# Kernel optimization log

Measured on AMD Instinct MI355X. Metric: run time of the kernel, lower is better.

The kernel has to match this reference:

```python
import jax, jax.numpy as jnp
import numpy as np

GN_GROUPS = 32
GN_EPS = 1e-5


def _conv3x3(x, w, b):
    # NCHW 3x3 conv, stride 1, pad 1
    y = jax.lax.conv_general_dilated(x, w, (1, 1), [(1, 1), (1, 1)],
                                     dimension_numbers=('NCHW', 'OIHW', 'NCHW'))
    return y + b[None, :, None, None]


def _bilinear(x, py, px):
    # x: [N,C,H,W]; py,px: [N,H,W] fractional sample coords; zeros outside.
    N, C, H, W = x.shape
    y0 = jnp.floor(py)
    x0 = jnp.floor(px)
    wy = py - y0
    wx = px - x0
    xf = x.reshape(N, C, H * W)
    out = jnp.zeros((N, C, H, W), x.dtype)
    corners = ((y0, x0, (1 - wy) * (1 - wx)),
               (y0, x0 + 1, (1 - wy) * wx),
               (y0 + 1, x0, wy * (1 - wx)),
               (y0 + 1, x0 + 1, wy * wx))
    for yy, xx, w in corners:
        valid = ((yy >= 0) & (yy <= H - 1) & (xx >= 0) & (xx <= W - 1)).astype(x.dtype)
        yi = jnp.clip(yy, 0, H - 1).astype(jnp.int32)
        xi = jnp.clip(xx, 0, W - 1).astype(jnp.int32)
        idx = (yi * W + xi).reshape(N, 1, H * W)
        g = jnp.take_along_axis(xf, idx, axis=2).reshape(N, C, H, W)
        out = out + g * (w * valid)[:, None]
    return out


def setup_inputs() -> dict:
    key = jax.random.key(0)
    ks = jax.random.split(key, 8)
    N, C, H, W = 4, 128, 160, 160
    s = 0.05
    return {
        'x': jax.random.normal(ks[0], (N, C, H, W), jnp.float32),
        'w_tm': jax.random.normal(ks[1], (4, C, 3, 3), jnp.float32) * s,
        'b_tm': jax.random.normal(ks[2], (4,), jnp.float32) * s,
        'w_tr': jax.random.normal(ks[3], (2, C, 3, 3), jnp.float32) * s,
        'b_tr': jax.random.normal(ks[4], (2,), jnp.float32) * s,
        'w_dcn': jax.random.normal(ks[5], (C, C, 3, 3), jnp.float32) * s,
        'gn_gamma': jnp.ones((C,), jnp.float32),
        'gn_beta': jnp.zeros((C,), jnp.float32),
    }


def reference(x, w_tm, b_tm, w_tr, b_tr, w_dcn, gn_gamma, gn_beta):
    N, C, H, W = x.shape
    Cout = w_dcn.shape[0]
    # regular 3x3 grid offsets: row0 = ky, row1 = kx, k ordered ky-major
    R = jnp.array([[-1., -1., -1., 0., 0., 0., 1., 1., 1.],
                   [-1., 0., 1., -1., 0., 1., -1., 0., 1.]], x.dtype)
    tm = _conv3x3(x, w_tm, b_tm)   # [N,4,H,W] -> per-pixel 2x2 affine
    tr = _conv3x3(x, w_tr, b_tr)   # [N,2,H,W] -> per-pixel (dy,dx) translation
    tmm = tm.transpose(0, 2, 3, 1).reshape(N, H, W, 2, 2)
    off = jnp.einsum('nhwij,jk->nhwik', tmm, R) - R  # [N,H,W,2,9]
    dy = off[:, :, :, 0, :] + tr[:, 0][..., None]    # [N,H,W,9]
    dx = off[:, :, :, 1, :] + tr[:, 1][..., None]
    hh = jnp.arange(H, dtype=x.dtype)[None, :, None, None]
    ww = jnp.arange(W, dtype=x.dtype)[None, None, :, None]
    kk = jnp.arange(9)
    ky = (kk // 3).astype(x.dtype)
    kx = (kk % 3).astype(x.dtype)
    py = hh - 1.0 + ky + dy  # stride=1, pad=1, dilation=1
    px = ww - 1.0 + kx + dx
    wk = w_dcn.reshape(Cout, C, 9)
    out = jnp.zeros((N, Cout, H, W), x.dtype)
    for k in range(9):  # fixed small loop over kernel points
        s = _bilinear(x, py[..., k], px[..., k])
        out = out + jnp.einsum('nchw,oc->nohw', s, wk[:, :, k])
    # GroupNorm
    og = out.reshape(N, GN_GROUPS, (Cout // GN_GROUPS) * H * W)
    mu = og.mean(axis=2, keepdims=True)
    var = og.var(axis=2, keepdims=True)
    og = (og - mu) * jax.lax.rsqrt(var + GN_EPS)
    out = og.reshape(N, Cout, H, W) * gn_gamma[None, :, None, None] + gn_beta[None, :, None, None]
    return jax.nn.relu(out + x)
```

## Files before the change

### kernel.cpp

```cpp
#include <hip/hip_runtime.h>
#include <hip/hip_fp16.h>
#include <math.h>

#define Hh 160
#define Ww 160
#define Cc 128
#define HW 25600
#define NPIX 102400

typedef __attribute__((ext_vector_type(8))) _Float16 half8;
typedef __attribute__((ext_vector_type(4))) float f32x4;
typedef __attribute__((ext_vector_type(4))) unsigned int u32x4;

union h2u { __half2 h; unsigned int u; };

#define WS_OFFS 0u
#define WS_WA   7372800u
#define WS_GSUM 7667712u
#define WS_GSQ  7668224u
#define WS_XT   7668736u
#define WS_RAW  33883136u

__global__ void wtrans_kernel(const float* __restrict__ w_dcn,
                              unsigned short* __restrict__ wA) {
    int idx = blockIdx.x * 256 + threadIdx.x;
    if (idx >= 9 * 128 * 128) return;
    int k = idx >> 14;
    int o = (idx >> 7) & 127;
    int c = idx & 127;
    wA[idx] = __half_as_ushort(__float2half(w_dcn[(o * 128 + c) * 9 + k]));
}

__global__ void __launch_bounds__(256) xpose_kernel(
    const float* __restrict__ x, unsigned short* __restrict__ xT) {
    __shared__ float L[128 * 65];
    int b = blockIdx.x;
    int n = b / 400;
    int px0 = (b - n * 400) * 64;
    int t = threadIdx.x;
    const float* xn = x + (size_t)n * Cc * HW + px0;
#pragma unroll
    for (int i = 0; i < 32; ++i) {
        int idx = i * 256 + t;
        int ch = idx >> 6;
        int pxl = idx & 63;
        L[ch * 65 + pxl] = xn[(size_t)ch * HW + pxl];
    }
    __syncthreads();
    unsigned short* dst = xT + ((size_t)n * HW + px0) * 128;
#pragma unroll
    for (int j = 0; j < 16; ++j) {
        int idx = j * 256 + t;
        int pxl = idx >> 6;
        int cp = idx & 63;
        h2u cv;
        cv.h = __floats2half2_rn(L[(2 * cp) * 65 + pxl],
                                 L[(2 * cp + 1) * 65 + pxl]);
        *(unsigned int*)(dst + (size_t)pxl * 128 + cp * 2) = cv.u;
    }
}

__global__ void __launch_bounds__(256) offs_kernel(
    const float* __restrict__ x, const float* __restrict__ w_tm,
    const float* __restrict__ b_tm, const float* __restrict__ w_tr,
    const float* __restrict__ b_tr, float* __restrict__ offs2) {
    __shared__ float wt[128 * 9 * 8];
    int t = threadIdx.x;
    for (int idx = t; idx < 6912; idx += 256) {
        int j = idx % 6;
        int rest = idx / 6;
        int tap = rest % 9;
        int c = rest / 9;
        float v = (j < 4) ? w_tm[(j * 128 + c) * 9 + tap]
                          : w_tr[((j - 4) * 128 + c) * 9 + tap];
        wt[rest * 8 + j] = v;
    }
    __syncthreads();
    int bid = blockIdx.x;
    int blk = (bid & 7) * 50 + (bid >> 3);
    int p = blk * 256 + t;
    int n = p / HW;
    int hw = p - n * HW;
    int h = hw / Ww;
    int w = hw - h * Ww;
    int addr[9];
    float msk[9];
#pragma unroll
    for (int tap = 0; tap < 9; ++tap) {
        int dy = tap / 3 - 1, dx = tap % 3 - 1;
        int yy = h + dy, xx = w + dx;
        bool v = (yy >= 0) && (yy < Hh) && (xx >= 0) && (xx < Ww);
        addr[tap] = v ? yy * Ww + xx : 0;
        msk[tap] = v ? 1.f : 0.f;
    }
    float a0 = 0, a1 = 0, a2 = 0, a3 = 0, a4 = 0, a5 = 0;
    const float* xn = x + n * Cc * HW;
#pragma unroll 2
    for (int c = 0; c < Cc; ++c) {
        const float* xc = xn + c * HW;
#pragma unroll
        for (int tap = 0; tap < 9; ++tap) {
            float v = msk[tap] * xc[addr[tap]];
            const float* wp = &wt[(c * 9 + tap) * 8];
            float4 w4 = *(const float4*)wp;
            float2 w2 = *(const float2*)(wp + 4);
            a0 += v * w4.x; a1 += v * w4.y; a2 += v * w4.z; a3 += v * w4.w;
            a4 += v * w2.x; a5 += v * w2.y;
        }
    }
    a0 += b_tm[0]; a1 += b_tm[1]; a2 += b_tm[2]; a3 += b_tm[3];
    a4 += b_tr[0]; a5 += b_tr[1];
#pragma unroll
    for (int k = 0; k < 9; ++k) {
        float r0 = (float)(k / 3) - 1.f;
        float r1 = (float)(k % 3) - 1.f;
        float2 st;
        st.x = (float)h + a0 * r0 + a1 * r1 + a4;
        st.y = (float)w + a2 * r0 + a3 * r1 + a5;
        *(float2*)(offs2 + ((size_t)k * NPIX + p) * 2) = st;
    }
}

__global__ void __launch_bounds__(256, 2) dcn2_kernel(
    const unsigned short* __restrict__ xT, const float* __restrict__ offs2,
    const unsigned short* __restrict__ wA, float* __restrict__ raw,
    float* __restrict__ gsum, float* __restrict__ gsq) {
    __shared__ __align__(16) unsigned short Bt[128 * 128];
    int t = threadIdx.x;
    int lane = t & 63;
    int wid = t >> 6;
    int wm = wid & 1, wn = wid >> 1;
    int quad = lane >> 4, l15 = lane & 15;
    int sub = lane >> 4;
    int s = lane & 15;

    int bid = blockIdx.x;
    int blk = (bid & 7) * 100 + (bid >> 3);
    int px0 = blk * 128;
    int n = px0 / HW;
    int hw0 = px0 - n * HW;
    const unsigned short* xb = xT + (size_t)n * HW * 128;
    const char* Ag = (const char*)wA;
    const float2* offv = (const float2*)offs2;
    int pbase = px0 + wid * 32 + sub;
    int sb = s << 3;

    f32x4 acc[4][4];
#pragma unroll
    for (int i = 0; i < 4; ++i)
#pragma unroll
        for (int j = 0; j < 4; ++j) acc[i][j] = (f32x4)0.f;

    float2 pc[8];
#pragma unroll
    for (int r = 0; r < 8; ++r)
        pc[r] = offv[(size_t)0 * NPIX + pbase + r * 4];

    for (int k = 0; k < 9; ++k) {
        __syncthreads();

        float2 pcn[8];
        if (k < 8) {
#pragma unroll
            for (int r = 0; r < 8; ++r)
                pcn[r] = offv[(size_t)(k + 1) * NPIX + pbase + r * 4];
        }

#pragma unroll
        for (int r = 0; r < 8; ++r) {
            int p = wid * 32 + r * 4 + sub;
            float py = pc[r].x, pxx = pc[r].y;
            float y0f = floorf(py), x0f = floorf(pxx);
            float fy = py - y0f, fx = pxx - x0f;
            int y0 = (int)y0f, xi0 = (int)x0f;
            int y1 = y0 + 1, xi1 = xi0 + 1;
            float w00 = (1.f - fy) * (1.f - fx), w01 = (1.f - fy) * fx;
            float w10 = fy * (1.f - fx), w11 = fy * fx;
            bool vy0 = (unsigned)y0 < (unsigned)Hh;
            bool vy1 = (unsigned)y1 < (unsigned)Hh;
            bool vx0 = (unsigned)xi0 < (unsigned)Ww;
            bool vx1 = (unsigned)xi1 < (unsigned)Ww;
            w00 = (vy0 && vx0) ? w00 : 0.f;
            w01 = (vy0 && vx1) ? w01 : 0.f;
            w10 = (vy1 && vx0) ? w10 : 0.f;
            w11 = (vy1 && vx1) ? w11 : 0.f;
            int cy0 = vy0 ? y0 : 0, cy1 = vy1 ? y1 : 0;
            int cx0 = vx0 ? xi0 : 0, cx1 = vx1 ? xi1 : 0;
            u32x4 v00 = *(const u32x4*)(xb + ((size_t)(cy0 * Ww + cx0) << 7) + sb);
            u32x4 v01 = *(const u32x4*)(xb + ((size_t)(cy0 * Ww + cx1) << 7) + sb);
            u32x4 v10 = *(const u32x4*)(xb + ((size_t)(cy1 * Ww + cx0) << 7) + sb);
            u32x4 v11 = *(const u32x4*)(xb + ((size_t)(cy1 * Ww + cx1) << 7) + sb);
            __half2 W00 = __float2half2_rn(w00);
            __half2 W01 = __float2half2_rn(w01);
            __half2 W10 = __float2half2_rn(w10);
            __half2 W11 = __float2half2_rn(w11);
            u32x4 outv;
#pragma unroll
            for (int e = 0; e < 4; ++e) {
                h2u a, b, c, d, o;
                a.u = v00[e]; b.u = v01[e]; c.u = v10[e]; d.u = v11[e];
                __half2 acc2 = __hmul2(W11, d.h);
                acc2 = __hfma2(W10, c.h, acc2);
                acc2 = __hfma2(W01, b.h, acc2);
                acc2 = __hfma2(W00, a.h, acc2);
                o.h = acc2;
                outv[e] = o.u;
            }
            *(u32x4*)&Bt[p * 128 + ((s ^ (p & 15)) << 3)] = outv;
        }
        __syncthreads();

#pragma unroll
        for (int q = 0; q < 4; ++q) {
            half8 a[4], b[4];
#pragma unroll
            for (int i = 0; i < 4; ++i)
                a[i] = *(const half8*)(Ag +
                        ((size_t)(k * 128 + wm * 64 + i * 16 + l15) << 8) +
                        q * 64 + quad * 16);
#pragma unroll
            for (int j = 0; j < 4; ++j) {
                int row = wn * 64 + j * 16 + l15;
                int ur = (q * 4 + quad) ^ (row & 15);
                b[j] = *(const half8*)&Bt[row * 128 + ur * 8];
            }
#pragma unroll
            for (int i = 0; i < 4; ++i)
#pragma unroll
                for (int j = 0; j < 4; ++j)
                    acc[i][j] = __builtin_amdgcn_mfma_f32_16x16x32_f16(
                        a[i], b[j], acc[i][j], 0, 0, 0);
        }

        if (k < 8) {
#pragma unroll
            for (int r = 0; r < 8; ++r) pc[r] = pcn[r];
        }
    }

    size_t rbase = ((size_t)n * Cc) * HW + hw0;
#pragma unroll
    for (int i = 0; i < 4; ++i) {
        float s_i = 0.f, q_i = 0.f;
#pragma unroll
        for (int j = 0; j < 4; ++j) {
            int pxl = wn * 64 + j * 16 + l15;
#pragma unroll
            for (int rr = 0; rr < 4; ++rr) {
                int o = wm * 64 + i * 16 + quad * 4 + rr;
                float v = acc[i][j][rr];
                raw[rbase + (size_t)o * HW + pxl] = v;
                s_i += v;
                q_i += v * v;
            }
        }
#pragma unroll
        for (int m = 1; m < 16; m <<= 1) {
            s_i += __shfl_xor(s_i, m);
            q_i += __shfl_xor(q_i, m);
        }
        if (l15 == 0) {
            int g = wm * 16 + i * 4 + quad;
            atomicAdd(&gsum[n * 32 + g], s_i);
            atomicAdd(&gsq[n * 32 + g], q_i);
        }
    }
}

__global__ void __launch_bounds__(256) finish_kernel(
    const float* __restrict__ raw, const float* __restrict__ x,
    const float* __restrict__ gsum, const float* __restrict__ gsq,
    const float* __restrict__ gamma, const float* __restrict__ beta,
    float* __restrict__ out) {
    int i = blockIdx.x * 256 + threadIdx.x;
    int e = i * 4;
    int n = e / (Cc * HW);
    int rem = e - n * (Cc * HW);
    int c = rem / HW;
    int g = c >> 2;
    const float inv = 1.f / 102400.f;
    float mu = gsum[n * 32 + g] * inv;
    float var = gsq[n * 32 + g] * inv - mu * mu;
    float rs = rsqrtf(var + 1e-5f);
    float sc = gamma[c] * rs;
    float sh = beta[c] - mu * sc;
    float4 v = *(const float4*)&raw[e];
    float4 xv = *(const float4*)&x[e];
    float4 r;
    r.x = fmaxf(v.x * sc + sh + xv.x, 0.f);
    r.y = fmaxf(v.y * sc + sh + xv.y, 0.f);
    r.z = fmaxf(v.z * sc + sh + xv.z, 0.f);
    r.w = fmaxf(v.w * sc + sh + xv.w, 0.f);
    *(float4*)&out[e] = r;
}

extern "C" void kernel_launch(void* const* d_in, const int* in_sizes, int n_in,
                              void* d_out, int out_size, void* d_ws, size_t ws_size,
                              hipStream_t stream) {
    const float* x      = (const float*)d_in[0];
    const float* w_tm   = (const float*)d_in[1];
    const float* b_tm   = (const float*)d_in[2];
    const float* w_tr   = (const float*)d_in[3];
    const float* b_tr   = (const float*)d_in[4];
    const float* w_dcn  = (const float*)d_in[5];
    const float* gamma  = (const float*)d_in[6];
    const float* beta   = (const float*)d_in[7];
    char* ws = (char*)d_ws;
    float*          offs2 = (float*)(ws + WS_OFFS);
    unsigned short* wA    = (unsigned short*)(ws + WS_WA);
    float*          gsum  = (float*)(ws + WS_GSUM);
    float*          gsq   = (float*)(ws + WS_GSQ);
    unsigned short* xT    = (unsigned short*)(ws + WS_XT);
    float*          raw   = (float*)(ws + WS_RAW);
    float* out = (float*)d_out;

    (void)hipMemsetAsync(gsum, 0, 1024, stream);
    wtrans_kernel<<<576, 256, 0, stream>>>(w_dcn, wA);
    xpose_kernel<<<1600, 256, 0, stream>>>(x, xT);
    offs_kernel<<<400, 256, 0, stream>>>(x, w_tm, b_tm, w_tr, b_tr, offs2);
    dcn2_kernel<<<800, 256, 0, stream>>>(xT, offs2, wA, raw, gsum, gsq);
    finish_kernel<<<12800, 256, 0, stream>>>(raw, x, gsum, gsq, gamma, beta, out);
}
```

Before: 329.2 us.

## Double-buffer bilinear gather tile and halve pixel tile per block

Cuts the DCN GEMM tile from 128 to 64 pixels per block, doubling the grid and raising launch-bounds occupancy to 5 blocks per CU. Splits the bilinear sampling into an issue phase (gathers held in registers) and a combine/LDS-write phase over a double-buffered LDS tile. The gathers for kernel point k+1 are then in flight while the MFMA loop runs on point k, with one barrier per iteration. This is meant to hide gather latency and improve occupancy, at the cost of loading the weight A-fragments twice as often per pixel and higher register pressure from the staged gathers.

```diff
diff --git a/kernel.cpp b/kernel.cpp
--- a/kernel.cpp
+++ b/kernel.cpp
@@ -121,11 +121,11 @@
     }
 }
 
-__global__ void __launch_bounds__(256, 2) dcn2_kernel(
+__global__ void __launch_bounds__(256, 5) dcn2_kernel(
     const unsigned short* __restrict__ xT, const float* __restrict__ offs2,
     const unsigned short* __restrict__ wA, float* __restrict__ raw,
     float* __restrict__ gsum, float* __restrict__ gsq) {
-    __shared__ __align__(16) unsigned short Bt[128 * 128];
+    __shared__ __align__(16) unsigned short Bt[2 * 64 * 128];
     int t = threadIdx.x;
     int lane = t & 63;
     int wid = t >> 6;
@@ -135,70 +135,66 @@
     int s = lane & 15;
 
     int bid = blockIdx.x;
-    int blk = (bid & 7) * 100 + (bid >> 3);
-    int px0 = blk * 128;
+    int blk = (bid & 7) * 200 + (bid >> 3);
+    int px0 = blk * 64;
     int n = px0 / HW;
     int hw0 = px0 - n * HW;
     const unsigned short* xb = xT + (size_t)n * HW * 128;
     const char* Ag = (const char*)wA;
     const float2* offv = (const float2*)offs2;
-    int pbase = px0 + wid * 32 + sub;
+    int pbase = px0 + wid * 16 + sub;
     int sb = s << 3;
 
-    f32x4 acc[4][4];
+    f32x4 acc[4][2];
 #pragma unroll
     for (int i = 0; i < 4; ++i)
 #pragma unroll
-        for (int j = 0; j < 4; ++j) acc[i][j] = (f32x4)0.f;
-
-    float2 pc[8];
-#pragma unroll
-    for (int r = 0; r < 8; ++r)
-        pc[r] = offv[(size_t)0 * NPIX + pbase + r * 4];
-
-    for (int k = 0; k < 9; ++k) {
-        __syncthreads();
-
-        float2 pcn[8];
-        if (k < 8) {
-#pragma unroll
-            for (int r = 0; r < 8; ++r)
-                pcn[r] = offv[(size_t)(k + 1) * NPIX + pbase + r * 4];
-        }
-
-#pragma unroll
-        for (int r = 0; r < 8; ++r) {
-            int p = wid * 32 + r * 4 + sub;
+        for (int j = 0; j < 2; ++j) acc[i][j] = (f32x4)0.f;
+
+    float2 pc[4], pcn[4];
+    u32x4 v00[4], v01[4], v10[4], v11[4];
+    float w00[4], w01[4], w10[4], w11[4];
+
+    auto issue = [&]() {
+#pragma unroll
+        for (int r = 0; r < 4; ++r) {
             float py = pc[r].x, pxx = pc[r].y;
             float y0f = floorf(py), x0f = floorf(pxx);
             float fy = py - y0f, fx = pxx - x0f;
             int y0 = (int)y0f, xi0 = (int)x0f;
             int y1 = y0 + 1, xi1 = xi0 + 1;
-            float w00 = (1.f - fy) * (1.f - fx), w01 = (1.f - fy) * fx;
-            float w10 = fy * (1.f - fx), w11 = fy * fx;
+            float a = (1.f - fy) * (1.f - fx), b = (1.f - fy) * fx;
+            float c = fy * (1.f - fx), d = fy * fx;
             bool vy0 = (unsigned)y0 < (unsigned)Hh;
             bool vy1 = (unsigned)y1 < (unsigned)Hh;
             bool vx0 = (unsigned)xi0 < (unsigned)Ww;
             bool vx1 = (unsigned)xi1 < (unsigned)Ww;
-            w00 = (vy0 && vx0) ? w00 : 0.f;
-            w01 = (vy0 && vx1) ? w01 : 0.f;
-            w10 = (vy1 && vx0) ? w10 : 0.f;
-            w11 = (vy1 && vx1) ? w11 : 0.f;
+            w00[r] = (vy0 && vx0) ? a : 0.f;
+            w01[r] = (vy0 && vx1) ? b : 0.f;
+            w10[r] = (vy1 && vx0) ? c : 0.f;
+            w11[r] = (vy1 && vx1) ? d : 0.f;
             int cy0 = vy0 ? y0 : 0, cy1 = vy1 ? y1 : 0;
             int cx0 = vx0 ? xi0 : 0, cx1 = vx1 ? xi1 : 0;
-            u32x4 v00 = *(const u32x4*)(xb + ((size_t)(cy0 * Ww + cx0) << 7) + sb);
-            u32x4 v01 = *(const u32x4*)(xb + ((size_t)(cy0 * Ww + cx1) << 7) + sb);
-            u32x4 v10 = *(const u32x4*)(xb + ((size_t)(cy1 * Ww + cx0) << 7) + sb);
-            u32x4 v11 = *(const u32x4*)(xb + ((size_t)(cy1 * Ww + cx1) << 7) + sb);
-            __half2 W00 = __float2half2_rn(w00);
-            __half2 W01 = __float2half2_rn(w01);
-            __half2 W10 = __float2half2_rn(w10);
-            __half2 W11 = __float2half2_rn(w11);
+            v00[r] = *(const u32x4*)(xb + ((size_t)(cy0 * Ww + cx0) << 7) + sb);
+            v01[r] = *(const u32x4*)(xb + ((size_t)(cy0 * Ww + cx1) << 7) + sb);
+            v10[r] = *(const u32x4*)(xb + ((size_t)(cy1 * Ww + cx0) << 7) + sb);
+            v11[r] = *(const u32x4*)(xb + ((size_t)(cy1 * Ww + cx1) << 7) + sb);
+        }
+    };
+
+    auto combine_write = [&](int bufbase) {
+#pragma unroll
+        for (int r = 0; r < 4; ++r) {
+            int p = wid * 16 + r * 4 + sub;
+            __half2 W00 = __float2half2_rn(w00[r]);
+            __half2 W01 = __float2half2_rn(w01[r]);
+            __half2 W10 = __float2half2_rn(w10[r]);
+            __half2 W11 = __float2half2_rn(w11[r]);
             u32x4 outv;
 #pragma unroll
             for (int e = 0; e < 4; ++e) {
                 h2u a, b, c, d, o;
-                a.u = v00[e]; b.u = v01[e]; c.u = v10[e]; d.u = v11[e];
+                a.u = v00[r][e]; b.u = v01[r][e]; c.u = v10[r][e]; d.u = v11[r][e];
                 __half2 acc2 = __hmul2(W11, d.h);
                 acc2 = __hfma2(W10, c.h, acc2);
                 acc2 = __hfma2(W01, b.h, acc2);
@@ -206,35 +202,55 @@
                 o.h = acc2;
                 outv[e] = o.u;
             }
-            *(u32x4*)&Bt[p * 128 + ((s ^ (p & 15)) << 3)] = outv;
-        }
-        __syncthreads();
+            *(u32x4*)&Bt[bufbase + p * 128 + ((s ^ (p & 15)) << 3)] = outv;
+        }
+    };
+
+#pragma unroll
+    for (int r = 0; r < 4; ++r) pc[r] = offv[pbase + r * 4];
+    issue();
+#pragma unroll
+    for (int r = 0; r < 4; ++r) pc[r] = offv[(size_t)1 * NPIX + pbase + r * 4];
+    combine_write(0);
+    __syncthreads();
+
+    for (int k = 0; k < 9; ++k) {
+        int bufr = (k & 1) * (64 * 128);
+        int bufw = ((k + 1) & 1) * (64 * 128);
+        if (k < 7) {
+#pragma unroll
+            for (int r = 0; r < 4; ++r)
+                pcn[r] = offv[(size_t)(k + 2) * NPIX + pbase + r * 4];
+        }
+        if (k < 8) issue();
 
 #pragma unroll
         for (int q = 0; q < 4; ++q) {
-            half8 a[4], b[4];
+            half8 a[4], b[2];
 #pragma unroll
             for (int i = 0; i < 4; ++i)
                 a[i] = *(const half8*)(Ag +
                         ((size_t)(k * 128 + wm * 64 + i * 16 + l15) << 8) +
                         q * 64 + quad * 16);
 #pragma unroll
-            for (int j = 0; j < 4; ++j) {
-                int row = wn * 64 + j * 16 + l15;
+            for (int j = 0; j < 2; ++j) {
+                int row = wn * 32 + j * 16 + l15;
                 int ur = (q * 4 + quad) ^ (row & 15);
-                b[j] = *(const half8*)&Bt[row * 128 + ur * 8];
+                b[j] = *(const half8*)&Bt[bufr + row * 128 + ur * 8];
             }
 #pragma unroll
             for (int i = 0; i < 4; ++i)
 #pragma unroll
-                for (int j = 0; j < 4; ++j)
+                for (int j = 0; j < 2; ++j)
                     acc[i][j] = __builtin_amdgcn_mfma_f32_16x16x32_f16(
                         a[i], b[j], acc[i][j], 0, 0, 0);
         }
 
-        if (k < 8) {
-#pragma unroll
-            for (int r = 0; r < 8; ++r) pc[r] = pcn[r];
+        if (k < 8) combine_write(bufw);
+        __syncthreads();
+        if (k < 7) {
+#pragma unroll
+            for (int r = 0; r < 4; ++r) pc[r] = pcn[r];
         }
     }
 
@@ -243,8 +259,8 @@
     for (int i = 0; i < 4; ++i) {
         float s_i = 0.f, q_i = 0.f;
 #pragma unroll
-        for (int j = 0; j < 4; ++j) {
-            int pxl = wn * 64 + j * 16 + l15;
+        for (int j = 0; j < 2; ++j) {
+            int pxl = wn * 32 + j * 16 + l15;
 #pragma unroll
             for (int rr = 0; rr < 4; ++rr) {
                 int o = wm * 64 + i * 16 + quad * 4 + rr;
@@ -318,6 +334,6 @@
     wtrans_kernel<<<576, 256, 0, stream>>>(w_dcn, wA);
     xpose_kernel<<<1600, 256, 0, stream>>>(x, xT);
     offs_kernel<<<400, 256, 0, stream>>>(x, w_tm, b_tm, w_tr, b_tr, offs2);
-    dcn2_kernel<<<800, 256, 0, stream>>>(xT, offs2, wA, raw, gsum, gsq);
+    dcn2_kernel<<<1600, 256, 0, stream>>>(xT, offs2, wA, raw, gsum, gsq);
     finish_kernel<<<12800, 256, 0, stream>>>(raw, x, gsum, gsq, gamma, beta, out);
 }
```

Result: slower. 399.9 us (+21.5%).

## Split fused bilinear-sampling GEMM into separate gather kernel and MFMA GEMM kernel

Applied to the files above, without the earlier changes.

Adds a bilin_kernel that precomputes all nine bilinearly sampled fp16 columns into a large workspace buffer, and a dcn3_kernel that runs the MFMA GEMM straight from global memory, with no LDS staging and no per-k barriers. The goal is to separate the latency-bound gather from the compute-bound GEMM so each can run at higher occupancy. The cost is writing and then reading about 236 MB of intermediate data. The split path is taken only when the workspace is large enough; otherwise the old fused kernel runs.

```diff
diff --git a/kernel.cpp b/kernel.cpp
--- a/kernel.cpp
+++ b/kernel.cpp
@@ -20,6 +20,9 @@
 #define WS_GSQ  7668224u
 #define WS_XT   7668736u
 #define WS_RAW  33883136u
+#define WS_B    86311936u
+#define WS_B_BYTES 235929600ull
+#define WS_END_SPLIT (86311936ull + 235929600ull)
 
 __global__ void wtrans_kernel(const float* __restrict__ w_dcn,
                               unsigned short* __restrict__ wA) {
@@ -121,6 +124,159 @@
     }
 }
 
+__global__ void __launch_bounds__(256, 4) bilin_kernel(
+    const unsigned short* __restrict__ xT, const float* __restrict__ offs2,
+    unsigned short* __restrict__ Bg) {
+    int t = threadIdx.x;
+    int lane = t & 63;
+    int wid = t >> 6;
+    int sub = lane >> 4;
+    int s = lane & 15;
+
+    int bid = blockIdx.x;
+    int blk = (bid & 7) * 200 + (bid >> 3);
+    int px0 = blk * 64;
+    int n = px0 / HW;
+    const unsigned short* xb = xT + (size_t)n * HW * 128;
+    const float2* offv = (const float2*)offs2;
+    int pbase = px0 + wid * 16 + sub;
+    int sb = s << 3;
+
+    u32x4 v00[2], v01[2], v10[2], v11[2];
+    float w00[2], w01[2], w10[2], w11[2];
+
+#define PREP(sl, kk, rr) do {                                               \
+    float2 pc_ = offv[(size_t)(kk) * NPIX + pbase + (rr) * 4];              \
+    float py_ = pc_.x, px_ = pc_.y;                                         \
+    float y0f_ = floorf(py_), x0f_ = floorf(px_);                           \
+    float fy_ = py_ - y0f_, fx_ = px_ - x0f_;                               \
+    int y0_ = (int)y0f_, xi0_ = (int)x0f_;                                  \
+    int y1_ = y0_ + 1, xi1_ = xi0_ + 1;                                     \
+    float wa_ = (1.f - fy_) * (1.f - fx_), wb_ = (1.f - fy_) * fx_;         \
+    float wc_ = fy_ * (1.f - fx_), wd_ = fy_ * fx_;                         \
+    bool vy0_ = (unsigned)y0_ < (unsigned)Hh;                               \
+    bool vy1_ = (unsigned)y1_ < (unsigned)Hh;                               \
+    bool vx0_ = (unsigned)xi0_ < (unsigned)Ww;                              \
+    bool vx1_ = (unsigned)xi1_ < (unsigned)Ww;                              \
+    w00[sl] = (vy0_ && vx0_) ? wa_ : 0.f;                                   \
+    w01[sl] = (vy0_ && vx1_) ? wb_ : 0.f;                                   \
+    w10[sl] = (vy1_ && vx0_) ? wc_ : 0.f;                                   \
+    w11[sl] = (vy1_ && vx1_) ? wd_ : 0.f;                                   \
+    int cy0_ = vy0_ ? y0_ : 0, cy1_ = vy1_ ? y1_ : 0;                       \
+    int cx0_ = vx0_ ? xi0_ : 0, cx1_ = vx1_ ? xi1_ : 0;                     \
+    v00[sl] = *(const u32x4*)(xb + ((size_t)(cy0_ * Ww + cx0_) << 7) + sb); \
+    v01[sl] = *(const u32x4*)(xb + ((size_t)(cy0_ * Ww + cx1_) << 7) + sb); \
+    v10[sl] = *(const u32x4*)(xb + ((size_t)(cy1_ * Ww + cx0_) << 7) + sb); \
+    v11[sl] = *(const u32x4*)(xb + ((size_t)(cy1_ * Ww + cx1_) << 7) + sb); \
+} while (0)
+
+#define EMIT(sl, kk, rr) do {                                               \
+    __half2 W00_ = __float2half2_rn(w00[sl]);                               \
+    __half2 W01_ = __float2half2_rn(w01[sl]);                               \
+    __half2 W10_ = __float2half2_rn(w10[sl]);                               \
+    __half2 W11_ = __float2half2_rn(w11[sl]);                               \
+    u32x4 outv_;                                                            \
+    _Pragma("unroll")                                                       \
+    for (int e = 0; e < 4; ++e) {                                           \
+        h2u a_, b_, c_, d_, o_;                                             \
+        a_.u = v00[sl][e]; b_.u = v01[sl][e];                               \
+        c_.u = v10[sl][e]; d_.u = v11[sl][e];                               \
+        __half2 t_ = __hmul2(W11_, d_.h);                                   \
+        t_ = __hfma2(W10_, c_.h, t_);                                       \
+        t_ = __hfma2(W01_, b_.h, t_);                                       \
+        t_ = __hfma2(W00_, a_.h, t_);                                       \
+        o_.h = t_;                                                          \
+        outv_[e] = o_.u;                                                    \
+    }                                                                       \
+    *(u32x4*)&Bg[((size_t)(kk) * NPIX + pbase + (rr) * 4) * 128 + sb]       \
+        = outv_;                                                            \
+} while (0)
+
+    for (int k = 0; k < 9; ++k) {
+        PREP(0, k, 0); PREP(1, k, 1);
+        EMIT(0, k, 0); PREP(0, k, 2);
+        EMIT(1, k, 1); PREP(1, k, 3);
+        EMIT(0, k, 2); EMIT(1, k, 3);
+    }
+#undef PREP
+#undef EMIT
+}
+
+__global__ void __launch_bounds__(256, 3) dcn3_kernel(
+    const unsigned short* __restrict__ Bg, const unsigned short* __restrict__ wA,
+    float* __restrict__ raw, float* __restrict__ gsum, float* __restrict__ gsq) {
+    int t = threadIdx.x;
+    int lane = t & 63;
+    int wid = t >> 6;
+    int wm = wid & 1, wn = wid >> 1;
+    int quad = lane >> 4, l15 = lane & 15;
+
+    int bid = blockIdx.x;
+    int blk = (bid & 7) * 100 + (bid >> 3);
+    int px0 = blk * 128;
+    int n = px0 / HW;
+    int hw0 = px0 - n * HW;
+    const char* Ag = (const char*)wA;
+    const char* Bb = (const char*)Bg;
+
+    f32x4 acc[4][4];
+#pragma unroll
+    for (int i = 0; i < 4; ++i)
+#pragma unroll
+        for (int j = 0; j < 4; ++j) acc[i][j] = (f32x4)0.f;
+
+    for (int k = 0; k < 9; ++k) {
+#pragma unroll
+        for (int q = 0; q < 4; ++q) {
+            half8 a[4], b[4];
+#pragma unroll
+            for (int i = 0; i < 4; ++i)
+                a[i] = *(const half8*)(Ag +
+                        ((size_t)(k * 128 + wm * 64 + i * 16 + l15) << 8) +
+                        q * 64 + quad * 16);
+#pragma unroll
+            for (int j = 0; j < 4; ++j) {
+                size_t prow = (size_t)k * NPIX + px0 + wn * 64 + j * 16 + l15;
+                b[j] = *(const half8*)(Bb + (prow << 8) + (q * 4 + quad) * 16);
+            }
+#pragma unroll
+            for (int i = 0; i < 4; ++i)
+#pragma unroll
+                for (int j = 0; j < 4; ++j)
+                    acc[i][j] = __builtin_amdgcn_mfma_f32_16x16x32_f16(
+                        a[i], b[j], acc[i][j], 0, 0, 0);
+        }
+    }
+
+    size_t rbase = ((size_t)n * Cc) * HW + hw0;
+#pragma unroll
+    for (int i = 0; i < 4; ++i) {
+        float s_i = 0.f, q_i = 0.f;
+#pragma unroll
+        for (int j = 0; j < 4; ++j) {
+            int pxl = wn * 64 + j * 16 + l15;
+#pragma unroll
+            for (int rr = 0; rr < 4; ++rr) {
+                int o = wm * 64 + i * 16 + quad * 4 + rr;
+                float v = acc[i][j][rr];
+                raw[rbase + (size_t)o * HW + pxl] = v;
+                s_i += v;
+                q_i += v * v;
+            }
+        }
+#pragma unroll
+        for (int m = 1; m < 16; m <<= 1) {
+            s_i += __shfl_xor(s_i, m);
+            q_i += __shfl_xor(q_i, m);
+        }
+        if (l15 == 0) {
+            int g = wm * 16 + i * 4 + quad;
+            atomicAdd(&gsum[n * 32 + g], s_i);
+            atomicAdd(&gsq[n * 32 + g], q_i);
+        }
+    }
+}
+
 __global__ void __launch_bounds__(256, 2) dcn2_kernel(
     const unsigned short* __restrict__ xT, const float* __restrict__ offs2,
     const unsigned short* __restrict__ wA, float* __restrict__ raw,
@@ -154,18 +310,16 @@
     float2 pc[8];
 #pragma unroll
     for (int r = 0; r < 8; ++r)
-        pc[r] = offv[(size_t)0 * NPIX + pbase + r * 4];
+        pc[r] = offv[pbase + r * 4];
 
     for (int k = 0; k < 9; ++k) {
         __syncthreads();
-
         float2 pcn[8];
         if (k < 8) {
 #pragma unroll
             for (int r = 0; r < 8; ++r)
                 pcn[r] = offv[(size_t)(k + 1) * NPIX + pbase + r * 4];
         }
-
 #pragma unroll
         for (int r = 0; r < 8; ++r) {
             int p = wid * 32 + r * 4 + sub;
@@ -312,12 +466,18 @@
     float*          gsq   = (float*)(ws + WS_GSQ);
     unsigned short* xT    = (unsigned short*)(ws + WS_XT);
     float*          raw   = (float*)(ws + WS_RAW);
+    unsigned short* Bg    = (unsigned short*)(ws + WS_B);
     float* out = (float*)d_out;
 
     (void)hipMemsetAsync(gsum, 0, 1024, stream);
     wtrans_kernel<<<576, 256, 0, stream>>>(w_dcn, wA);
     xpose_kernel<<<1600, 256, 0, stream>>>(x, xT);
     offs_kernel<<<400, 256, 0, stream>>>(x, w_tm, b_tm, w_tr, b_tr, offs2);
-    dcn2_kernel<<<800, 256, 0, stream>>>(xT, offs2, wA, raw, gsum, gsq);
+    if (ws_size >= WS_END_SPLIT) {
+        bilin_kernel<<<1600, 256, 0, stream>>>(xT, offs2, Bg);
+        dcn3_kernel<<<800, 256, 0, stream>>>(Bg, wA, raw, gsum, gsq);
+    } else {
+        dcn2_kernel<<<800, 256, 0, stream>>>(xT, offs2, wA, raw, gsum, gsq);
+    }
     finish_kernel<<<12800, 256, 0, stream>>>(raw, x, gsum, gsq, gamma, beta, out);
 }
```

Result: no change. 332.5 us (+1.0%).
